# Optimization experiments

Measured on AMD Instinct MI355X. Metric: run time of the kernel, lower is better.

Reference implementation:

```python
import jax, jax.numpy as jnp
import numpy as np

MAX_RADIUS = 2.0
NUM_BASIS = 30
HIDDEN = 100
BETA = 5.0

# e3nn rescaled_act.Softplus(beta): softplus rescaled so E[sp(randn)^2] == 1.
_x = np.random.RandomState(0).randn(1_000_000)
_sp = np.logaddexp(0.0, BETA * _x) / BETA
SP_FACTOR = float(1.0 / np.sqrt((_sp ** 2).mean()))

# o3.irreducible_basis_to_xyz(): permutation mapping l=1 irreducible order (y, z, x) -> (x, y, z)
IRREP_TO_XYZ = jnp.array([[0.0, 0.0, 1.0], [1.0, 0.0, 0.0], [0.0, 1.0, 0.0]], dtype=jnp.float32)


def act(x):
    # torch.nn.functional.softplus(x, beta) * factor
    return jax.nn.softplus(BETA * x) * (SP_FACTOR / BETA)


def setup_inputs() -> dict:
    key = jax.random.key(0)
    k0, k1, k2, k3, k4 = jax.random.split(key, 5)
    Z, A = 2, 1024
    features = jax.random.normal(k0, (Z, A, 1), dtype=jnp.float32)
    # scale so a good fraction of pairwise distances are inside the radial cutoff (max_radius=2)
    geometry = jax.random.normal(k1, (Z, A, 3), dtype=jnp.float32) * 0.5
    W0 = jax.random.normal(k2, (NUM_BASIS, HIDDEN), dtype=jnp.float32)
    W1 = jax.random.normal(k3, (HIDDEN, HIDDEN), dtype=jnp.float32)
    W2 = jax.random.normal(k4, (HIDDEN, 1), dtype=jnp.float32)
    return {"features": features, "geometry": geometry, "W0": W0, "W1": W1, "W2": W2}


def reference(features, geometry, W0, W1, W2):
    # features: [z, a, 1] (scalar, l=0); geometry: [z, a, 3]
    rel = geometry[:, None, :, :] - geometry[:, :, None, :]  # [z, a, b, 3] (r_b - r_a)
    r2 = jnp.sum(rel * rel, axis=-1)                          # [z, a, b]
    mask = r2 > 1e-12                                         # self-pairs excluded (l=1 SH undefined at 0)
    r = jnp.where(mask, jnp.sqrt(jnp.where(mask, r2, 1.0)), 0.0)

    # CosineBasisModel: soft cosine bumps on [0, max_radius], then FC MLP (L=2 hidden, weight-norm / sqrt(fan_in))
    step = MAX_RADIUS / (NUM_BASIS - 1)
    centers = jnp.linspace(0.0, MAX_RADIUS, NUM_BASIS)
    d = (r[..., None] - centers) / step                       # [z, a, b, NUM_BASIS]
    basis = jnp.where(jnp.abs(d) < 1.0, jnp.cos(0.5 * jnp.pi * d) ** 2, 0.0)
    h = act(basis @ (W0 / np.sqrt(NUM_BASIS)))
    h = act(h @ (W1 / np.sqrt(HIDDEN)))
    R = (h @ (W2 / np.sqrt(HIDDEN)))[..., 0]                  # radial weight per pair [z, a, b]

    # l=1 real spherical harmonics, irreducible order (y, z, x), component-normalized by sqrt(3)
    unit = rel / jnp.where(mask, r, 1.0)[..., None]
    Y = jnp.sqrt(3.0) * jnp.stack([unit[..., 1], unit[..., 2], unit[..., 0]], axis=-1)
    Y = jnp.where(mask[..., None], Y, 0.0)                    # [z, a, b, 3]

    # Convolution: out[z,a,i] = sum_b K[z,a,b,i,0] * features[z,b,0], K = R * Y
    out = jnp.einsum('zabi,zab,zb->zai', Y, R, features[..., 0])
    # trailing basis change to xyz
    return jnp.einsum('ij,zaj->zai', IRREP_TO_XYZ, out)
```

## Files before the change

### kernel.cpp

```cpp
#include <hip/hip_runtime.h>
#include <cstdint>
#include <cmath>

#define T_TAB 1024
#define NB 30
#define NH 100
#define ZDIM 2
#define ADIM 1024
#define APB  4
#define RMAX_D (60.0/29.0)

#define SPF5 0.28125f

__device__ __forceinline__ float actf(float x) {
    float y = 5.0f * x;
    float mx = fmaxf(y, 0.0f);
    return (mx + log1pf(expf(-fabsf(y)))) * SPF5;
}

__global__ __launch_bounds__(128) void build_table_kernel(
    const float* __restrict__ W0, const float* __restrict__ W1,
    const float* __restrict__ W2, float* __restrict__ tab, float hstep)
{
    __shared__ float sh0[NH];
    __shared__ float rpart[2];
    const int j = threadIdx.x;
    const int k = (int)blockIdx.x - 1;
    const float r = (float)k * hstep;
    const float stepf = (float)(2.0 / 29.0);

    float s = 0.0f;
    if (j < NH) {
        int i0 = (int)floorf(r / stepf);
        #pragma unroll
        for (int t = 0; t < 4; t++) {
            int i = i0 - 1 + t;
            if (i >= 0 && i < NB) {
                float c = (float)((double)i * (2.0 / 29.0));
                float d = (r - c) / stepf;
                if (fabsf(d) < 1.0f) {
                    float cs = cosf(1.5707964f * d);
                    s = fmaf(cs * cs, W0[i * NH + j], s);
                }
            }
        }
        sh0[j] = actf(s * 0.18257418583505536f);
    }
    __syncthreads();

    float scj = 0.0f;
    if (j < NH) {
        float a0 = 0.0f, a1 = 0.0f, a2 = 0.0f, a3 = 0.0f;
        #pragma unroll
        for (int q = 0; q < NH; q += 4) {
            a0 = fmaf(sh0[q + 0], W1[(q + 0) * NH + j], a0);
            a1 = fmaf(sh0[q + 1], W1[(q + 1) * NH + j], a1);
            a2 = fmaf(sh0[q + 2], W1[(q + 2) * NH + j], a2);
            a3 = fmaf(sh0[q + 3], W1[(q + 3) * NH + j], a3);
        }
        float h1 = actf(((a0 + a1) + (a2 + a3)) * 0.1f);
        scj = h1 * (W2[j] * 0.1f);
    }

    float v = scj;
    #pragma unroll
    for (int off = 32; off > 0; off >>= 1) v += __shfl_down(v, off, 64);
    if ((j & 63) == 0) rpart[j >> 6] = v;
    __syncthreads();
    if (j == 0) tab[blockIdx.x] = rpart[0] + rpart[1];
}

__global__ __launch_bounds__(256) void pair_kernel(
    const float* __restrict__ feat, const float* __restrict__ geo,
    const float* __restrict__ tab, float* __restrict__ out)
{
    __shared__ float4 ltab4[T_TAB - 1];
    __shared__ float sgeo[ADIM * 3];
    __shared__ float sfeat[ADIM];

    const int z = blockIdx.y;
    const int tid = threadIdx.x;

    const float* geoz  = geo  + z * ADIM * 3;
    const float* featz = feat + z * ADIM;
    for (int i = tid; i < T_TAB - 1; i += 256) {
        ltab4[i] = make_float4(tab[i], tab[i + 1], tab[i + 2], tab[i + 3]);
    }
    const float rtail = tab[T_TAB + 1];
    for (int i = tid; i < ADIM * 3;  i += 256) sgeo[i] = geoz[i];
    for (int i = tid; i < ADIM;      i += 256) sfeat[i] = featz[i];
    __syncthreads();

    const int wv = tid >> 6, lane = tid & 63;
    const int a = blockIdx.x * APB + wv;
    const float ax = sgeo[a * 3 + 0], ay = sgeo[a * 3 + 1], az = sgeo[a * 3 + 2];
    const float inv_h = (float)((double)(T_TAB - 1) / RMAX_D);
    const float rmaxf = (float)RMAX_D;
    const float sqrt3 = 1.7320508075688772f;

    float accx = 0.0f, accy = 0.0f, accz = 0.0f;
    #pragma unroll 4
    for (int k = 0; k < ADIM / 64; k++) {
        const int b = k * 64 + lane;
        float dx = sgeo[b * 3 + 0] - ax;
        float dy = sgeo[b * 3 + 1] - ay;
        float dz = sgeo[b * 3 + 2] - az;
        float r2 = fmaf(dx, dx, fmaf(dy, dy, dz * dz));
        if (r2 > 1e-12f) {
            float rinv = rsqrtf(r2);
            float r = r2 * rinv;
            float R;
            if (r < rmaxf) {
                float x = r * inv_h;
                int i = (int)x;
                if (i > T_TAB - 2) i = T_TAB - 2;
                float u = x - (float)i;
                float4 p = ltab4[i];
                R = p.y + 0.5f * u * ((p.z - p.x) +
                        u * ((2.0f * p.x - 5.0f * p.y + 4.0f * p.z - p.w) +
                        u * (3.0f * (p.y - p.z) + p.w - p.x)));
            } else {
                R = rtail;
            }
            float w = sqrt3 * R * sfeat[b] * rinv;
            accx = fmaf(dx, w, accx);
            accy = fmaf(dy, w, accy);
            accz = fmaf(dz, w, accz);
        }
    }

    #pragma unroll
    for (int off = 32; off > 0; off >>= 1) {
        accx += __shfl_down(accx, off, 64);
        accy += __shfl_down(accy, off, 64);
        accz += __shfl_down(accz, off, 64);
    }
    if (lane == 0) {
        float* o = out + ((size_t)z * ADIM + a) * 3;
        o[0] = accx; o[1] = accy; o[2] = accz;
    }
}

extern "C" void kernel_launch(void* const* d_in, const int* in_sizes, int n_in,
                              void* d_out, int out_size, void* d_ws, size_t ws_size,
                              hipStream_t stream) {
    const float* feat = (const float*)d_in[0];
    const float* geo  = (const float*)d_in[1];
    const float* W0   = (const float*)d_in[2];
    const float* W1   = (const float*)d_in[3];
    const float* W2   = (const float*)d_in[4];
    float* out = (float*)d_out;
    float* tab = (float*)d_ws;
    (void)in_sizes; (void)n_in; (void)out_size; (void)ws_size;

    const float hstep = (float)(RMAX_D / (double)(T_TAB - 1));

    build_table_kernel<<<dim3(T_TAB + 2), dim3(128), 0, stream>>>(W0, W1, W2, tab, hstep);
    pair_kernel<<<dim3(ADIM / APB, ZDIM), dim3(256), 0, stream>>>(feat, geo, tab, out);
}
```

Baseline: 18.08 us.

## Shrink radial lookup table, pack two nodes per block, vectorize staging loads

Cuts the cubic-interpolation table for the radial MLP from 1024 to 256 nodes and computes two table nodes per 256-thread block, so the table-build kernel launches far fewer blocks. The pair kernel's shared-memory staging of geometry and features now uses float4 loads, and its table staging moves less data. The coarser table adds interpolation error to the radial weights, which may loosen accuracy against the reference.

```diff
diff --git a/kernel.cpp b/kernel.cpp
--- a/kernel.cpp
+++ b/kernel.cpp
@@ -2,7 +2,8 @@
 #include <cstdint>
 #include <cmath>
 
-#define T_TAB 1024
+#define T_TAB 256
+#define NNODE (T_TAB + 2)
 #define NB 30
 #define NH 100
 #define ZDIM 2
@@ -18,19 +19,21 @@
     return (mx + log1pf(expf(-fabsf(y)))) * SPF5;
 }
 
-__global__ __launch_bounds__(128) void build_table_kernel(
+__global__ __launch_bounds__(256) void build_table_kernel(
     const float* __restrict__ W0, const float* __restrict__ W1,
     const float* __restrict__ W2, float* __restrict__ tab, float hstep)
 {
-    __shared__ float sh0[NH];
-    __shared__ float rpart[2];
-    const int j = threadIdx.x;
-    const int k = (int)blockIdx.x - 1;
-    const float r = (float)k * hstep;
+    __shared__ float sh0[2][NH];
+    __shared__ float rpart[4];
+    const int tid = threadIdx.x;
+    const int half = tid >> 7;
+    const int j = tid & 127;
+    const int node = 2 * blockIdx.x + half;
+    const float r = (float)(node - 1) * hstep;
     const float stepf = (float)(2.0 / 29.0);
 
-    float s = 0.0f;
     if (j < NH) {
+        float s = 0.0f;
         int i0 = (int)floorf(r / stepf);
         #pragma unroll
         for (int t = 0; t < 4; t++) {
@@ -44,7 +47,7 @@
                 }
             }
         }
-        sh0[j] = actf(s * 0.18257418583505536f);
+        sh0[half][j] = actf(s * 0.18257418583505536f);
     }
     __syncthreads();
 
@@ -53,21 +56,21 @@
         float a0 = 0.0f, a1 = 0.0f, a2 = 0.0f, a3 = 0.0f;
         #pragma unroll
         for (int q = 0; q < NH; q += 4) {
-            a0 = fmaf(sh0[q + 0], W1[(q + 0) * NH + j], a0);
-            a1 = fmaf(sh0[q + 1], W1[(q + 1) * NH + j], a1);
-            a2 = fmaf(sh0[q + 2], W1[(q + 2) * NH + j], a2);
-            a3 = fmaf(sh0[q + 3], W1[(q + 3) * NH + j], a3);
+            a0 = fmaf(sh0[half][q + 0], W1[(q + 0) * NH + j], a0);
+            a1 = fmaf(sh0[half][q + 1], W1[(q + 1) * NH + j], a1);
+            a2 = fmaf(sh0[half][q + 2], W1[(q + 2) * NH + j], a2);
+            a3 = fmaf(sh0[half][q + 3], W1[(q + 3) * NH + j], a3);
         }
         float h1 = actf(((a0 + a1) + (a2 + a3)) * 0.1f);
         scj = h1 * (W2[j] * 0.1f);
     }
-
     float v = scj;
     #pragma unroll
     for (int off = 32; off > 0; off >>= 1) v += __shfl_down(v, off, 64);
-    if ((j & 63) == 0) rpart[j >> 6] = v;
+    if ((tid & 63) == 0) rpart[tid >> 6] = v;
     __syncthreads();
-    if (j == 0) tab[blockIdx.x] = rpart[0] + rpart[1];
+    if ((tid & 127) == 0)
+        tab[node] = rpart[half << 1] + rpart[(half << 1) + 1];
 }
 
 __global__ __launch_bounds__(256) void pair_kernel(
@@ -75,20 +78,21 @@
     const float* __restrict__ tab, float* __restrict__ out)
 {
     __shared__ float4 ltab4[T_TAB - 1];
-    __shared__ float sgeo[ADIM * 3];
-    __shared__ float sfeat[ADIM];
+    __shared__ __align__(16) float sgeo[ADIM * 3];
+    __shared__ __align__(16) float sfeat[ADIM];
 
     const int z = blockIdx.y;
     const int tid = threadIdx.x;
 
     const float* geoz  = geo  + z * ADIM * 3;
     const float* featz = feat + z * ADIM;
-    for (int i = tid; i < T_TAB - 1; i += 256) {
+    for (int i = tid; i < T_TAB - 1; i += 256)
         ltab4[i] = make_float4(tab[i], tab[i + 1], tab[i + 2], tab[i + 3]);
-    }
     const float rtail = tab[T_TAB + 1];
-    for (int i = tid; i < ADIM * 3;  i += 256) sgeo[i] = geoz[i];
-    for (int i = tid; i < ADIM;      i += 256) sfeat[i] = featz[i];
+    for (int i = tid; i < (ADIM * 3) / 4; i += 256)
+        ((float4*)sgeo)[i] = ((const float4*)geoz)[i];
+    for (int i = tid; i < ADIM / 4; i += 256)
+        ((float4*)sfeat)[i] = ((const float4*)featz)[i];
     __syncthreads();
 
     const int wv = tid >> 6, lane = tid & 63;
@@ -155,6 +159,6 @@
 
     const float hstep = (float)(RMAX_D / (double)(T_TAB - 1));
 
-    build_table_kernel<<<dim3(T_TAB + 2), dim3(128), 0, stream>>>(W0, W1, W2, tab, hstep);
+    build_table_kernel<<<dim3(NNODE / 2), dim3(256), 0, stream>>>(W0, W1, W2, tab, hstep);
     pair_kernel<<<dim3(ADIM / APB, ZDIM), dim3(256), 0, stream>>>(feat, geo, tab, out);
 }
```

Result: faster. 15.63 us (-13.5%).
